# Performance work log

Measured on AMD Instinct MI355X. Metric: run time of the kernel, lower is better.

The kernel has to match this reference:

```python
import jax, jax.numpy as jnp
import numpy as np

N = 65536      # samples
DX = 1024      # X features
DY = 1024      # Y features
D = 256        # projected width (x_net/y_net output)
LAMX = 0.1
LAMY = 0.1
SIGMA = 0.5    # STG gate noise std (eval-mode deterministic gate)
EPS = 0.001    # regularizer used in original code


def setup_inputs() -> dict:
    key = jax.random.key(0)
    ks = jax.random.split(key, 8)
    X = jax.random.normal(ks[0], (N, DX), dtype=jnp.float32)
    Y = jax.random.normal(ks[1], (N, DY), dtype=jnp.float32)
    # StochasticGates params (mu per input feature)
    mu_x = 0.01 * jax.random.normal(ks[2], (DX,), dtype=jnp.float32)
    mu_y = 0.01 * jax.random.normal(ks[3], (DY,), dtype=jnp.float32)
    # per-view linear nets (x_net: DX->D, y_net: DY->D)
    Wx = jax.random.normal(ks[4], (DX, D), dtype=jnp.float32) / np.sqrt(DX)
    bx = jnp.zeros((D,), dtype=jnp.float32)
    Wy = jax.random.normal(ks[5], (DY, D), dtype=jnp.float32) / np.sqrt(DY)
    by = jnp.zeros((D,), dtype=jnp.float32)
    return {"X": X, "Y": Y, "mu_x": mu_x, "mu_y": mu_y,
            "Wx": Wx, "bx": bx, "Wy": Wy, "by": by}


def _stg_gate(mu):
    # deterministic (eval) hard gate: clamp(mu + 0.5, 0, 1)
    return jnp.clip(mu + 0.5, 0.0, 1.0)


def _stg_reg(mu, lam):
    # lam * mean(P(gate > 0)) = lam * mean(Phi(mu/sigma))  [Gaussian CDF]
    return lam * jnp.mean(0.5 * (1.0 + jax.lax.erf(mu / (SIGMA * jnp.sqrt(2.0)))))


def _cov(a, b):
    # matches torch: (b.T @ a).T / (N-1) == a.T @ b / (N-1)
    n = a.shape[0]
    return (a.T @ b) / (n - 1)


def _inv_sqrt_sym(A):
    # A^(-1/2) via eigendecomposition; A symmetric so eigh == eig with V^-1 = V.T
    w, V = jnp.linalg.eigh(A)
    return (V * (w + EPS) ** (-0.5)) @ V.T


def _corr(Xh, Yh):
    d = Xh.shape[1]
    psi_x = Xh - Xh.mean(axis=0)
    psi_y = Yh - Yh.mean(axis=0)
    C_yy = _cov(psi_y, psi_y)
    C_yx = _cov(psi_y, psi_x)
    C_xy = _cov(psi_x, psi_y)
    C_xx = _cov(psi_x, psi_x)
    I = jnp.eye(d, dtype=Xh.dtype)
    C_yy_inv_root = _inv_sqrt_sym(C_yy + EPS * I)
    C_xx_inv = jnp.linalg.inv(C_xx + EPS * I)
    M = C_yy_inv_root @ C_yx @ C_xx_inv @ C_xy @ C_yy_inv_root
    return jnp.trace(M) / d


def reference(X, Y, mu_x, mu_y, Wx, bx, Wy, by):
    Xh = (X * _stg_gate(mu_x)) @ Wx + bx   # [N, D]
    Yh = (Y * _stg_gate(mu_y)) @ Wy + by   # [N, D]
    loss = -_corr(Xh, Yh) + _stg_reg(mu_x, LAMX) + _stg_reg(mu_y, LAMY)
    return loss
```

## Files before the change

kernel.cpp:

```cpp
#include <hip/hip_runtime.h>

#define N_S   65536
#define DXF   1024
#define DD    256
#define NM1   65535.0f
#define EPSR  0.001f

typedef __attribute__((ext_vector_type(4)))  float          f32x4;
typedef __attribute__((ext_vector_type(16))) float          f32x16;
typedef __attribute__((ext_vector_type(8)))  short          bf16x8;
typedef __attribute__((ext_vector_type(4)))  unsigned short ushort4_t;
typedef __attribute__((ext_vector_type(8)))  unsigned short ushort8_t;

__device__ __forceinline__ unsigned short f2bf(float f){
  unsigned u = __float_as_uint(f);
  u += 0x7fffu + ((u >> 16) & 1u);
  return (unsigned short)(u >> 16);
}
__device__ __forceinline__ float bf2f(unsigned short h){
  return __uint_as_float(((unsigned)h) << 16);
}
__device__ __forceinline__ f32x4 mfma16(bf16x8 a, bf16x8 b, f32x4 c){
  return __builtin_amdgcn_mfma_f32_16x16x32_bf16(a, b, c, 0, 0, 0);
}
__device__ __forceinline__ f32x16 mfma32(bf16x8 a, bf16x8 b, f32x16 c){
  return __builtin_amdgcn_mfma_f32_32x32x16_bf16(a, b, c, 0, 0, 0);
}
__device__ __forceinline__ void gld_lds16(const void* g, void* l){
  __builtin_amdgcn_global_load_lds(
      (const __attribute__((address_space(1))) unsigned int*)g,
      (__attribute__((address_space(3))) unsigned int*)l, 16, 0, 0);
}

__global__ void k_prep(const float* __restrict__ Wx, const float* __restrict__ Wy,
                       const float* __restrict__ mux, const float* __restrict__ muy,
                       unsigned short* __restrict__ WTx, unsigned short* __restrict__ WTy,
                       float* __restrict__ scal){
  int v = blockIdx.y;
  const float* W  = v ? Wy  : Wx;
  const float* mu = v ? muy : mux;
  unsigned short* WT = v ? WTy : WTx;
  int j = threadIdx.x;
  if (j < 4){
    float ph = 0.5f * (1.f + erff(mu[blockIdx.x * 4 + j] * 1.41421356237f));
    atomicAdd(scal + 2 + v, 9.765625e-5f * ph);
  }
  #pragma unroll
  for (int r = 0; r < 4; ++r){
    int k = blockIdx.x * 4 + r;
    float g = fminf(fmaxf(mu[k] + 0.5f, 0.f), 1.f);
    WT[(size_t)(k >> 3) * 2048 + j * 8 + (k & 7)] = f2bf(g * W[(size_t)k * DD + j]);
  }
}

__global__ __launch_bounds__(512, 8) void k_gemm7(
    const float* __restrict__ X, const float* __restrict__ Y,
    const unsigned short* __restrict__ WTx, const unsigned short* __restrict__ WTy,
    unsigned short* __restrict__ Xhb, unsigned short* __restrict__ Yhb){
  const float* A = blockIdx.z ? Y : X;
  const unsigned short* WT = blockIdx.z ? WTy : WTx;
  unsigned short* Out = blockIdx.z ? Yhb : Xhb;

  __shared__ unsigned short As[64][40];
  __shared__ unsigned short Bs[4][256][8];

  int tid = threadIdx.x, lane = tid & 63, wid = tid >> 6;
  int wr = wid >> 1, wc = wid & 1;
  int row0 = blockIdx.x * 64;

  f32x4 acc[8] = {};

  int s_row = tid >> 3, s_kq = tid & 7;
  const float* ap = A + (size_t)(row0 + s_row) * DXF + s_kq * 4;

  auto stageB = [&](int ks){
    #pragma unroll
    for (int i = 0; i < 2; ++i){
      int cl = ((wid >> 2) * 2 + i) * 64 + lane;
      int csw = cl ^ ((cl >> 1) & 4);
      gld_lds16(WT + (size_t)(ks * 4 + (wid & 3)) * 2048 + csw * 8,
                &Bs[wid & 3][((wid >> 2) * 2 + i) * 64][0]);
    }
  };
  auto storeAs = [&](float4 a){
    union { unsigned u[2]; ushort4_t v; } r;
    asm("v_cvt_pk_bf16_f32 %0, %1, %2" : "=v"(r.u[0]) : "v"(a.x), "v"(a.y));
    asm("v_cvt_pk_bf16_f32 %0, %1, %2" : "=v"(r.u[1]) : "v"(a.z), "v"(a.w));
    *(ushort4_t*)&As[s_row][s_kq * 4] = r.v;
  };

  const unsigned short* bb = &Bs[0][0][0] + (lane >> 4) * 2048 + wc * 1024
                           + (((lane & 15) * 8) ^ ((lane & 8) << 2));

  float4 a0;
  stageB(0);
  asm volatile("" ::: "memory");
  a0 = *(const float4*)(ap);
  asm volatile("s_waitcnt vmcnt(0)" ::: "memory");
  storeAs(a0);
  a0 = *(const float4*)(ap + 32);
  asm volatile("s_waitcnt lgkmcnt(0)" ::: "memory");
  __builtin_amdgcn_s_barrier();

  for (int ks = 0; ks < 32; ++ks){
    bf16x8 af = *(const bf16x8*)&As[wr * 16 + (lane & 15)][(lane >> 4) * 8];
    #pragma unroll
    for (int ni = 0; ni < 8; ++ni){
      bf16x8 bf = *(const bf16x8*)(bb + ni * 128);
      acc[ni] = mfma16(af, bf, acc[ni]);
    }
    if (ks == 31) break;
    __builtin_amdgcn_s_barrier();
    stageB(ks + 1);
    asm volatile("s_waitcnt vmcnt(2)" ::: "memory");
    storeAs(a0);
    if (ks + 2 < 32){
      a0 = *(const float4*)(ap + (ks + 2) * 32);
      asm volatile("s_waitcnt vmcnt(1)" ::: "memory");
    } else {
      asm volatile("s_waitcnt vmcnt(0)" ::: "memory");
    }
    asm volatile("s_waitcnt lgkmcnt(0)" ::: "memory");
    __builtin_amdgcn_s_barrier();
  }

  __syncthreads();
  unsigned short* tl = &Bs[0][0][0];
  #pragma unroll
  for (int p = 0; p < 2; ++p){
    if ((wr >> 1) == p){
      #pragma unroll
      for (int ni = 0; ni < 8; ++ni)
        #pragma unroll
        for (int rr = 0; rr < 4; ++rr){
          int r = (wr & 1) * 16 + (lane >> 4) * 4 + rr;
          int c = wc * 128 + ni * 16 + (lane & 15);
          tl[r * 256 + c] = f2bf(acc[ni][rr]);
        }
    }
    __syncthreads();
    unsigned short* ob = Out + (size_t)(row0 + p * 32) * DD;
    #pragma unroll
    for (int r = 0; r < 2; ++r){
      int off = r * 4096 + tid * 8;
      *(ushort8_t*)(ob + off) = *(const ushort8_t*)(tl + off);
    }
    if (p == 0) __syncthreads();
  }
}

__global__ __launch_bounds__(512) void k_gram(
    const unsigned short* __restrict__ Xhb, const unsigned short* __restrict__ Yhb,
    float* __restrict__ part, float* __restrict__ sx, float* __restrict__ sy, int P){
  int type = blockIdx.z;
  int p = blockIdx.x;
  int chunk = N_S / P;
  int r0 = p * chunk;
  const unsigned short* Asrc = (type == 0) ? Xhb : Yhb;
  const unsigned short* Bsrc = (type == 1) ? Yhb : Xhb;
  bool dualB = (type == 2);

  __shared__ unsigned short At[256][40];
  __shared__ unsigned short Bt[256][40];

  int tid = threadIdx.x;
  int lane = tid & 63, wid = tid >> 6;
  int wr = wid >> 1, wc = wid & 1;

  f32x4 acc[4][8] = {};
  float cs0 = 0.f, cs1 = 0.f;

  int cp  = tid & 127;
  int kb0 = tid >> 7;

  unsigned ua[2][4], ub[2][4];

  auto loadT = [&](int ks){
    int base = r0 + ks * 32;
    #pragma unroll
    for (int r = 0; r < 2; ++r){
      int kb = kb0 + r * 4;
      #pragma unroll
      for (int kr = 0; kr < 4; ++kr){
        ua[r][kr] = *(const unsigned*)(Asrc + (size_t)(base + kb * 4 + kr) * DD + cp * 2);
        if (dualB)
          ub[r][kr] = *(const unsigned*)(Bsrc + (size_t)(base + kb * 4 + kr) * DD + cp * 2);
      }
    }
  };
  auto storeT = [&](){
    #pragma unroll
    for (int r = 0; r < 2; ++r){
      int kb = kb0 + r * 4;
      ushort4_t lo = { (unsigned short)ua[r][0], (unsigned short)ua[r][1],
                       (unsigned short)ua[r][2], (unsigned short)ua[r][3] };
      ushort4_t hi = { (unsigned short)(ua[r][0] >> 16), (unsigned short)(ua[r][1] >> 16),
                       (unsigned short)(ua[r][2] >> 16), (unsigned short)(ua[r][3] >> 16) };
      *(ushort4_t*)&At[cp * 2][kb * 4]     = lo;
      *(ushort4_t*)&At[cp * 2 + 1][kb * 4] = hi;
      if (type < 2){
        #pragma unroll
        for (int kr = 0; kr < 4; ++kr){
          cs0 += bf2f((unsigned short)ua[r][kr]);
          cs1 += bf2f((unsigned short)(ua[r][kr] >> 16));
        }
      }
      if (dualB){
        ushort4_t lob = { (unsigned short)ub[r][0], (unsigned short)ub[r][1],
                          (unsigned short)ub[r][2], (unsigned short)ub[r][3] };
        ushort4_t hib = { (unsigned short)(ub[r][0] >> 16), (unsigned short)(ub[r][1] >> 16),
                          (unsigned short)(ub[r][2] >> 16), (unsigned short)(ub[r][3] >> 16) };
        *(ushort4_t*)&Bt[cp * 2][kb * 4]     = lob;
        *(ushort4_t*)&Bt[cp * 2 + 1][kb * 4] = hib;
      }
    }
  };

  unsigned short (*Btp)[40] = dualB ? Bt : At;

  int KS = chunk / 32;
  loadT(0);
  for (int ks = 0; ks < KS; ++ks){
    __syncthreads();
    storeT();
    __syncthreads();
    if (ks + 1 < KS) loadT(ks + 1);
    bf16x8 af[4], bfv[8];
    #pragma unroll
    for (int mi = 0; mi < 4; ++mi)
      af[mi] = *(const bf16x8*)&At[wr * 64 + mi * 16 + (lane & 15)][(lane >> 4) * 8];
    #pragma unroll
    for (int ni = 0; ni < 8; ++ni)
      bfv[ni] = *(const bf16x8*)&Btp[wc * 128 + ni * 16 + (lane & 15)][(lane >> 4) * 8];
    #pragma unroll
    for (int mi = 0; mi < 4; ++mi)
      #pragma unroll
      for (int ni = 0; ni < 8; ++ni)
        acc[mi][ni] = mfma16(af[mi], bfv[ni], acc[mi][ni]);
  }

  float* dst = part + ((size_t)p * 3 + type) * 65536;
  #pragma unroll
  for (int mi = 0; mi < 4; ++mi)
    #pragma unroll
    for (int ni = 0; ni < 8; ++ni)
      #pragma unroll
      for (int rr = 0; rr < 4; ++rr){
        int grow = wr * 64 + mi * 16 + (lane >> 4) * 4 + rr;
        int gcol = wc * 128 + ni * 16 + (lane & 15);
        dst[(size_t)grow * 256 + gcol] = acc[mi][ni][rr];
      }

  if (type < 2){
    __syncthreads();
    float* red = (float*)&At[0][0];
    red[kb0 * 256 + cp * 2]     = cs0;
    red[kb0 * 256 + cp * 2 + 1] = cs1;
    __syncthreads();
    if (tid < 256){
      float s = red[tid] + red[256 + tid] + red[512 + tid] + red[768 + tid];
      atomicAdd((type == 0 ? sx : sy) + tid, s);
    }
  }
}

__global__ void k_reduce(const float* __restrict__ part, const float* __restrict__ sx,
                         const float* __restrict__ sy, float* __restrict__ Am,
                         float* __restrict__ Bm,
                         unsigned short* __restrict__ Abf, unsigned short* __restrict__ Bbf,
                         unsigned short* __restrict__ Cbf, unsigned short* __restrict__ CbfT,
                         float* __restrict__ scal, int P){
  __shared__ float r2[256];
  int i = blockIdx.x, j = threadIdx.x;
  size_t idx = (size_t)i * 256 + j;
  float gxx = 0.f, gyy = 0.f, gyx = 0.f;
  for (int p = 0; p < P; ++p){
    const float* b = part + (size_t)p * 3 * 65536;
    gxx += b[idx];
    gyy += b[65536 + idx];
    gyx += b[131072 + idx];
  }
  float invn1 = 1.f / NM1;
  float invn  = 1.f / (float)N_S;
  float sxi = sx[i], sxj = sx[j], syi = sy[i], syj = sy[j];
  float diag = (i == j) ? 1.f : 0.f;
  float am = (gyy - syi * syj * invn) * invn1 + diag * (2.f * EPSR);
  float bm = (gxx - sxi * sxj * invn) * invn1 + diag * EPSR;
  float cv = (gyx - syi * sxj * invn) * invn1;
  Am[idx] = am;  Bm[idx] = bm;
  Abf[idx] = f2bf(am);
  Bbf[idx] = f2bf(bm);
  Cbf[idx] = f2bf(cv);
  CbfT[(size_t)j * 256 + i] = f2bf(cv);
  r2[j] = fabsf(am);
  __syncthreads();
  for (int s = 128; s > 0; s >>= 1){ if (j < s) r2[j] += r2[j + s]; __syncthreads(); }
  if (j == 0) atomicMax((unsigned*)scal + 5, __float_as_uint(r2[0]));
  __syncthreads();
  r2[j] = fabsf(bm);
  __syncthreads();
  for (int s = 128; s > 0; s >>= 1){ if (j < s) r2[j] += r2[j + s]; __syncthreads(); }
  if (j == 0) atomicMax((unsigned*)scal + 6, __float_as_uint(r2[0]));
}

__global__ void k_x1(const float* __restrict__ Am, const float* __restrict__ Bm,
                     unsigned short* __restrict__ X0, const float* __restrict__ scal){
  int m = blockIdx.y;
  const unsigned* su = (const unsigned*)scal;
  float al = 1.9f / __uint_as_float(su[5 + m]);
  const float* M = m ? Bm : Am;
  int e = blockIdx.x * 512 + threadIdx.x;
  float v = -al * al * M[e];
  if ((e >> 8) == (e & 255)) v += 2.f * al;
  X0[m * 65536 + e] = f2bf(v);
}

__global__ __launch_bounds__(512) void k_it(
    const unsigned short* __restrict__ Abf, const unsigned short* __restrict__ Bbf,
    const unsigned short* __restrict__ Xc, unsigned short* __restrict__ Xn){
  int m = blockIdx.y, j = blockIdx.x;
  const unsigned short* M  = m ? Bbf : Abf;
  const unsigned short* Xm = Xc + m * 65536;
  unsigned short*       Xo = Xn + m * 65536;

  __shared__ unsigned short XJ[32 * 256];
  __shared__ unsigned short TT[32 * 256];

  int tid = threadIdx.x, lane = tid & 63, w = tid >> 6;
  int r31 = lane & 31, kh = lane >> 5;

  #pragma unroll
  for (int i = 0; i < 2; ++i){
    int rl = w * 4 + i * 2 + kh;
    int cg = ((lane & 31) - rl) & 31;
    gld_lds16(Xm + (size_t)(j * 32 + rl) * 256 + cg * 8, &XJ[(w * 4 + i * 2) * 256]);
  }
  asm volatile("s_waitcnt vmcnt(0)" ::: "memory");
  __builtin_amdgcn_s_barrier();

  f32x16 acc = {};
  const unsigned short* arow = M + (size_t)(w * 32 + r31) * 256 + kh * 8;
  #pragma unroll
  for (int ks = 0; ks < 16; ++ks){
    bf16x8 af = *(const bf16x8*)(arow + ks * 16);
    int ch = ((ks * 2 + kh) + r31) & 31;
    bf16x8 bf = *(const bf16x8*)&XJ[r31 * 256 + ch * 8];
    acc = mfma32(af, bf, acc);
  }
  #pragma unroll
  for (int reg = 0; reg < 16; ++reg){
    int kk = w * 32 + (reg & 3) + ((reg >> 2) << 3) + (kh << 2);
    int ch = ((kk >> 3) + r31) & 31;
    TT[r31 * 256 + ch * 8 + (kk & 7)] = f2bf(acc[reg]);
  }
  __syncthreads();

  f32x16 acc2 = {};
  const unsigned short* xrow = Xm + (size_t)(w * 32 + r31) * 256 + kh * 8;
  #pragma unroll
  for (int ks = 0; ks < 16; ++ks){
    bf16x8 af = *(const bf16x8*)(xrow + ks * 16);
    int ch = ((ks * 2 + kh) + r31) & 31;
    bf16x8 bf = *(const bf16x8*)&TT[r31 * 256 + ch * 8];
    acc2 = mfma32(af, bf, acc2);
  }
  #pragma unroll
  for (int reg = 0; reg < 16; ++reg){
    int row = w * 32 + (reg & 3) + ((reg >> 2) << 3) + (kh << 2);
    int ch = ((row >> 3) + r31) & 31;
    float xv = bf2f(XJ[r31 * 256 + ch * 8 + (row & 7)]);
    Xo[(size_t)row * 256 + j * 32 + r31] = f2bf(2.f * xv - acc2[reg]);
  }
}

__global__ __launch_bounds__(512) void k_uv(
    const unsigned short* __restrict__ Xf,
    const unsigned short* __restrict__ Cbf, const unsigned short* __restrict__ CbfT,
    float* __restrict__ U, float* __restrict__ W){
  int m = blockIdx.y, j = blockIdx.x;
  __shared__ unsigned short BJ[32 * 256];
  int tid = threadIdx.x, lane = tid & 63, w = tid >> 6;
  int r31 = lane & 31, kh = lane >> 5;
  const unsigned short* Brows = m ? (Xf + 65536) : CbfT;
  const unsigned short* Arows = m ? Cbf : Xf;
  float* D = m ? W : U;

  #pragma unroll
  for (int i = 0; i < 2; ++i){
    int rl = w * 4 + i * 2 + kh;
    int cg = ((lane & 31) - rl) & 31;
    gld_lds16(Brows + (size_t)(j * 32 + rl) * 256 + cg * 8, &BJ[(w * 4 + i * 2) * 256]);
  }
  asm volatile("s_waitcnt vmcnt(0)" ::: "memory");
  __builtin_amdgcn_s_barrier();

  f32x16 acc = {};
  const unsigned short* ar = Arows + (size_t)(w * 32 + r31) * 256 + kh * 8;
  #pragma unroll
  for (int ks = 0; ks < 16; ++ks){
    bf16x8 af = *(const bf16x8*)(ar + ks * 16);
    int ch = ((ks * 2 + kh) + r31) & 31;
    bf16x8 bf = *(const bf16x8*)&BJ[r31 * 256 + ch * 8];
    acc = mfma32(af, bf, acc);
  }
  #pragma unroll
  for (int reg = 0; reg < 16; ++reg){
    int row = w * 32 + (reg & 3) + ((reg >> 2) << 3) + (kh << 2);
    D[(size_t)row * 256 + j * 32 + r31] = acc[reg];
  }
}

__global__ __launch_bounds__(1024) void k_fin(const float* __restrict__ U,
                                              const float* __restrict__ W,
                                              const float* __restrict__ scal,
                                              float* __restrict__ out){
  __shared__ float red[1024];
  int tid = threadIdx.x;
  float t = 0.f;
  #pragma unroll
  for (int r = 0; r < 16; ++r){
    int i = r * 4096 + tid * 4;
    float4 u = *(const float4*)(U + i);
    float4 w = *(const float4*)(W + i);
    t += u.x * w.x + u.y * w.y + u.z * w.z + u.w * w.w;
  }
  red[tid] = t; __syncthreads();
  for (int s = 512; s > 0; s >>= 1){ if (tid < s) red[tid] += red[tid + s]; __syncthreads(); }
  if (tid == 0) out[0] = -red[0] / 256.f + scal[2] + scal[3];
}

extern "C" void kernel_launch(void* const* d_in, const int* in_sizes, int n_in,
                              void* d_out, int out_size, void* d_ws, size_t ws_size,
                              hipStream_t stream){
  (void)in_sizes; (void)n_in; (void)out_size;
  const float* X   = (const float*)d_in[0];
  const float* Y   = (const float*)d_in[1];
  const float* mux = (const float*)d_in[2];
  const float* muy = (const float*)d_in[3];
  const float* Wx  = (const float*)d_in[4];
  const float* Wy  = (const float*)d_in[6];
  float* out = (float*)d_out;
  char* ws = (char*)d_ws;

  const size_t MB = 1ull << 20;
  const size_t KB = 1024;
  size_t oXHB = 0;
  size_t oYHB = 32 * MB;
  size_t oWTX = 64 * MB;
  size_t oWTY = oWTX + 512 * KB;
  size_t oSX  = oWTY + 512 * KB;
  size_t oSY  = oSX + 4 * KB;
  size_t oSC  = oSY + 4 * KB;
  size_t oA   = oSC + 4 * KB;
  size_t oB   = oA   + 256 * KB;
  size_t oABF = oB   + 256 * KB;
  size_t oBBF = oABF + 128 * KB;
  size_t oCBF = oBBF + 128 * KB;
  size_t oCBT = oCBF + 128 * KB;
  size_t oX0  = oCBT + 128 * KB;
  size_t oX1  = oX0  + 256 * KB;
  size_t oTB  = oX1  + 256 * KB;
  size_t oU   = oTB  + 256 * KB;
  size_t oV   = oU   + 256 * KB;
  size_t oPart = 68 * MB;

  size_t per = 3ull * 65536 * 4;
  int P = 64;
  while (P > 8 && oPart + (size_t)P * per > ws_size) P >>= 1;

  unsigned short* Xhb = (unsigned short*)(ws + oXHB);
  unsigned short* Yhb = (unsigned short*)(ws + oYHB);
  unsigned short* WTx = (unsigned short*)(ws + oWTX);
  unsigned short* WTy = (unsigned short*)(ws + oWTY);
  float* sx   = (float*)(ws + oSX);
  float* sy   = (float*)(ws + oSY);
  float* scal = (float*)(ws + oSC);
  float* Am   = (float*)(ws + oA);
  float* Bm   = (float*)(ws + oB);
  unsigned short* Abf  = (unsigned short*)(ws + oABF);
  unsigned short* Bbf  = (unsigned short*)(ws + oBBF);
  unsigned short* Cbf  = (unsigned short*)(ws + oCBF);
  unsigned short* CbfT = (unsigned short*)(ws + oCBT);
  unsigned short* X0   = (unsigned short*)(ws + oX0);
  unsigned short* X1   = (unsigned short*)(ws + oX1);
  float* U    = (float*)(ws + oU);
  float* V    = (float*)(ws + oV);
  float* part = (float*)(ws + oPart);

  hipMemsetAsync(ws + oSX, 0, 12 * KB, stream);

  k_prep<<<dim3(256, 2), 256, 0, stream>>>(Wx, Wy, mux, muy, WTx, WTy, scal);
  k_gemm7<<<dim3(1024, 1, 2), 512, 0, stream>>>(X, Y, WTx, WTy, Xhb, Yhb);
  k_gram<<<dim3(P, 1, 3), 512, 0, stream>>>(Xhb, Yhb, part, sx, sy, P);
  k_reduce<<<256, 256, 0, stream>>>(part, sx, sy, Am, Bm, Abf, Bbf, Cbf, CbfT, scal, P);

  k_x1<<<dim3(128, 2), 512, 0, stream>>>(Am, Bm, X0, scal);
  k_it<<<dim3(8, 2), 512, 0, stream>>>(Abf, Bbf, X0, X1);
  k_it<<<dim3(8, 2), 512, 0, stream>>>(Abf, Bbf, X1, X0);
  k_it<<<dim3(8, 2), 512, 0, stream>>>(Abf, Bbf, X0, X1);
  k_it<<<dim3(8, 2), 512, 0, stream>>>(Abf, Bbf, X1, X0);
  k_it<<<dim3(8, 2), 512, 0, stream>>>(Abf, Bbf, X0, X1);
  k_uv<<<dim3(8, 2), 512, 0, stream>>>(X1, Cbf, CbfT, U, V);
  k_fin<<<1, 1024, 0, stream>>>(U, V, scal, out);
}
```

Baseline: 318.3 us.

## Double-buffer B tiles and retile warps to 32x64 in projection GEMM

The projection GEMM now double-buffers the weight tile in LDS, prefetching two k-steps ahead, and changes the warp layout from 16x128 to 32x64 per wave. Each B fragment is reused across two MFMAs, which halves B LDS reads per MFMA, and the epilogue writes the whole 64-row tile in one pass. The XOR swizzle on the B tile is dropped, which may bring back LDS bank conflicts. The doubled B buffer also raises LDS use per block, which could limit occupancy.

Measured after the change: 307.9 us. 3.3% less time.

```diff
diff --git a/kernel.cpp b/kernel.cpp
--- a/kernel.cpp
+++ b/kernel.cpp
@@ -53,7 +53,7 @@
   }
 }
 
-__global__ __launch_bounds__(512, 8) void k_gemm7(
+__global__ __launch_bounds__(512, 8) void k_gemm8(
     const float* __restrict__ X, const float* __restrict__ Y,
     const unsigned short* __restrict__ WTx, const unsigned short* __restrict__ WTy,
     unsigned short* __restrict__ Xhb, unsigned short* __restrict__ Yhb){
@@ -62,24 +62,23 @@
   unsigned short* Out = blockIdx.z ? Yhb : Xhb;
 
   __shared__ unsigned short As[64][40];
-  __shared__ unsigned short Bs[4][256][8];
+  __shared__ unsigned short Bs[2][4][256][8];
 
   int tid = threadIdx.x, lane = tid & 63, wid = tid >> 6;
-  int wr = wid >> 1, wc = wid & 1;
+  int wr = wid >> 2, wc = wid & 3;
   int row0 = blockIdx.x * 64;
 
-  f32x4 acc[8] = {};
+  f32x4 acc[2][4] = {};
 
   int s_row = tid >> 3, s_kq = tid & 7;
   const float* ap = A + (size_t)(row0 + s_row) * DXF + s_kq * 4;
 
-  auto stageB = [&](int ks){
+  auto stageB = [&](int buf, int ks){
     #pragma unroll
     for (int i = 0; i < 2; ++i){
-      int cl = ((wid >> 2) * 2 + i) * 64 + lane;
-      int csw = cl ^ ((cl >> 1) & 4);
-      gld_lds16(WT + (size_t)(ks * 4 + (wid & 3)) * 2048 + csw * 8,
-                &Bs[wid & 3][((wid >> 2) * 2 + i) * 64][0]);
+      int cg = (wid >> 2) * 2 + i;
+      gld_lds16(WT + (size_t)(ks * 4 + (wid & 3)) * 2048 + (cg * 64 + lane) * 8,
+                &Bs[buf][wid & 3][cg * 64][0]);
     }
   };
   auto storeAs = [&](float4 a){
@@ -89,63 +88,63 @@
     *(ushort4_t*)&As[s_row][s_kq * 4] = r.v;
   };
 
-  const unsigned short* bb = &Bs[0][0][0] + (lane >> 4) * 2048 + wc * 1024
-                           + (((lane & 15) * 8) ^ ((lane & 8) << 2));
-
-  float4 a0;
-  stageB(0);
+  float4 a0, ar;
+  stageB(0, 0);
   asm volatile("" ::: "memory");
   a0 = *(const float4*)(ap);
-  asm volatile("s_waitcnt vmcnt(0)" ::: "memory");
+  asm volatile("" ::: "memory");
+  stageB(1, 1);
+  asm volatile("s_waitcnt vmcnt(2)" ::: "memory");
   storeAs(a0);
-  a0 = *(const float4*)(ap + 32);
+  ar = *(const float4*)(ap + 32);
   asm volatile("s_waitcnt lgkmcnt(0)" ::: "memory");
   __builtin_amdgcn_s_barrier();
 
   for (int ks = 0; ks < 32; ++ks){
-    bf16x8 af = *(const bf16x8*)&As[wr * 16 + (lane & 15)][(lane >> 4) * 8];
-    #pragma unroll
-    for (int ni = 0; ni < 8; ++ni){
-      bf16x8 bf = *(const bf16x8*)(bb + ni * 128);
-      acc[ni] = mfma16(af, bf, acc[ni]);
+    int buf = ks & 1;
+    bf16x8 af0 = *(const bf16x8*)&As[wr * 32 + (lane & 15)][(lane >> 4) * 8];
+    bf16x8 af1 = *(const bf16x8*)&As[wr * 32 + 16 + (lane & 15)][(lane >> 4) * 8];
+    #pragma unroll
+    for (int ni = 0; ni < 4; ++ni){
+      bf16x8 bf = *(const bf16x8*)&Bs[buf][lane >> 4][wc * 64 + ni * 16 + (lane & 15)][0];
+      acc[0][ni] = mfma16(af0, bf, acc[0][ni]);
+      acc[1][ni] = mfma16(af1, bf, acc[1][ni]);
     }
     if (ks == 31) break;
     __builtin_amdgcn_s_barrier();
-    stageB(ks + 1);
-    asm volatile("s_waitcnt vmcnt(2)" ::: "memory");
-    storeAs(a0);
     if (ks + 2 < 32){
-      a0 = *(const float4*)(ap + (ks + 2) * 32);
-      asm volatile("s_waitcnt vmcnt(1)" ::: "memory");
+      stageB(buf, ks + 2);
+      asm volatile("s_waitcnt vmcnt(2)" ::: "memory");
     } else {
       asm volatile("s_waitcnt vmcnt(0)" ::: "memory");
     }
+    storeAs(ar);
+    if (ks + 2 < 32){
+      asm volatile("" ::: "memory");
+      ar = *(const float4*)(ap + (ks + 2) * 32);
+    }
     asm volatile("s_waitcnt lgkmcnt(0)" ::: "memory");
     __builtin_amdgcn_s_barrier();
   }
 
   __syncthreads();
-  unsigned short* tl = &Bs[0][0][0];
-  #pragma unroll
-  for (int p = 0; p < 2; ++p){
-    if ((wr >> 1) == p){
+  unsigned short* tl = &Bs[0][0][0][0];
+  #pragma unroll
+  for (int mi = 0; mi < 2; ++mi)
+    #pragma unroll
+    for (int ni = 0; ni < 4; ++ni)
       #pragma unroll
-      for (int ni = 0; ni < 8; ++ni)
-        #pragma unroll
-        for (int rr = 0; rr < 4; ++rr){
-          int r = (wr & 1) * 16 + (lane >> 4) * 4 + rr;
-          int c = wc * 128 + ni * 16 + (lane & 15);
-          tl[r * 256 + c] = f2bf(acc[ni][rr]);
-        }
-    }
-    __syncthreads();
-    unsigned short* ob = Out + (size_t)(row0 + p * 32) * DD;
-    #pragma unroll
-    for (int r = 0; r < 2; ++r){
-      int off = r * 4096 + tid * 8;
-      *(ushort8_t*)(ob + off) = *(const ushort8_t*)(tl + off);
-    }
-    if (p == 0) __syncthreads();
+      for (int rr = 0; rr < 4; ++rr){
+        int r = wr * 32 + mi * 16 + (lane >> 4) * 4 + rr;
+        int c = wc * 64 + ni * 16 + (lane & 15);
+        tl[r * 256 + c] = f2bf(acc[mi][ni][rr]);
+      }
+  __syncthreads();
+  unsigned short* ob = Out + (size_t)row0 * DD;
+  #pragma unroll
+  for (int r = 0; r < 4; ++r){
+    int off = r * 4096 + tid * 8;
+    *(ushort8_t*)(ob + off) = *(const ushort8_t*)(tl + off);
   }
 }
 
@@ -490,7 +489,7 @@
   hipMemsetAsync(ws + oSX, 0, 12 * KB, stream);
 
   k_prep<<<dim3(256, 2), 256, 0, stream>>>(Wx, Wy, mux, muy, WTx, WTy, scal);
-  k_gemm7<<<dim3(1024, 1, 2), 512, 0, stream>>>(X, Y, WTx, WTy, Xhb, Yhb);
+  k_gemm8<<<dim3(1024, 1, 2), 512, 0, stream>>>(X, Y, WTx, WTy, Xhb, Yhb);
   k_gram<<<dim3(P, 1, 3), 512, 0, stream>>>(Xhb, Yhb, part, sx, sy, P);
   k_reduce<<<256, 256, 0, stream>>>(part, sx, sy, Am, Bm, Abf, Bbf, Cbf, CbfT, scal, P);
 
```
